# Kernel optimization log

Measured on AMD Instinct MI355X. Metric: run time of the kernel, lower is better.

## Reference

```python
import jax, jax.numpy as jnp
import numpy as np
import math

DIM = 1024
NUM_HEADS = 16
HEAD_DIM = DIM // NUM_HEADS  # 64
LAYER_IDX = 12
LAMBDA_INIT = 0.8 - 0.6 * math.exp(-0.3 * (LAYER_IDX - 1))
LN_EPS = 1e-5


def setup_inputs() -> dict:
    key = jax.random.key(0)
    ks = jax.random.split(key, 11)
    B, S = 2, 2048
    x = jax.random.normal(ks[0], (B, S, DIM), dtype=jnp.float32)
    s = 1.0 / math.sqrt(DIM)
    Wq = jax.random.normal(ks[1], (DIM, 2 * DIM), dtype=jnp.float32) * s
    Wk = jax.random.normal(ks[2], (DIM, 2 * DIM), dtype=jnp.float32) * s
    Wv = jax.random.normal(ks[3], (DIM, DIM), dtype=jnp.float32) * s
    Wo = jax.random.normal(ks[4], (DIM, DIM), dtype=jnp.float32) * s
    lambda_q1 = jax.random.normal(ks[5], (HEAD_DIM,), dtype=jnp.float32) * 0.1
    lambda_k1 = jax.random.normal(ks[6], (HEAD_DIM,), dtype=jnp.float32) * 0.1
    lambda_q2 = jax.random.normal(ks[7], (HEAD_DIM,), dtype=jnp.float32) * 0.1
    lambda_k2 = jax.random.normal(ks[8], (HEAD_DIM,), dtype=jnp.float32) * 0.1
    gamma = jnp.ones((DIM,), dtype=jnp.float32)
    beta = jnp.zeros((DIM,), dtype=jnp.float32)
    return {"x": x, "Wq": Wq, "Wk": Wk, "Wv": Wv, "Wo": Wo,
            "lambda_q1": lambda_q1, "lambda_k1": lambda_k1,
            "lambda_q2": lambda_q2, "lambda_k2": lambda_k2,
            "gamma": gamma, "beta": beta}


def reference(x, Wq, Wk, Wv, Wo, lambda_q1, lambda_k1, lambda_q2, lambda_k2, gamma, beta):
    B, S, _ = x.shape
    scaling = HEAD_DIM ** (-0.5)
    # projections: [B,S,H,2d] / [B,S,H,d] -> [B,H,S,*]
    Q = (x @ Wq).reshape(B, S, NUM_HEADS, 2 * HEAD_DIM).transpose(0, 2, 1, 3)
    K = (x @ Wk).reshape(B, S, NUM_HEADS, 2 * HEAD_DIM).transpose(0, 2, 1, 3)
    V = (x @ Wv).reshape(B, S, NUM_HEADS, HEAD_DIM).transpose(0, 2, 1, 3)
    # lambda scalar
    lamb = (jnp.exp(jnp.sum(lambda_q1 * lambda_k1))
            - jnp.exp(jnp.sum(lambda_q2 * lambda_k2)) + LAMBDA_INIT)
    Q1, Q2 = jnp.split(Q, 2, axis=-1)
    K1, K2 = jnp.split(K, 2, axis=-1)
    A1 = jnp.einsum('bhqd,bhkd->bhqk', Q1, K1) * scaling
    A2 = jnp.einsum('bhqd,bhkd->bhqk', Q2, K2) * scaling
    attn = jax.nn.softmax(A1, axis=-1) - lamb * jax.nn.softmax(A2, axis=-1)
    out = jnp.einsum('bhqk,bhkd->bhqd', attn, V)  # [B,H,S,d]
    out = out.transpose(0, 2, 1, 3).reshape(B, S, DIM)
    out = out @ Wo
    # LayerNorm
    mu = jnp.mean(out, axis=-1, keepdims=True)
    var = jnp.var(out, axis=-1, keepdims=True)
    out = (out - mu) * jax.lax.rsqrt(var + LN_EPS) * gamma + beta
    return out
```

## Files before the change

### kernel.cpp

```cpp
#include <hip/hip_runtime.h>
#include <hip/hip_bf16.h>

typedef short bf16x8 __attribute__((ext_vector_type(8)));
typedef float f32x4 __attribute__((ext_vector_type(4)));
typedef unsigned short us4v __attribute__((ext_vector_type(4)));
typedef unsigned int uint2v __attribute__((ext_vector_type(2)));

#define DEV static __device__ __forceinline__

DEV float bf2f(unsigned short u){ unsigned int x = ((unsigned int)u)<<16; float f; __builtin_memcpy(&f,&x,4); return f; }
DEV unsigned short f2bf(float f){ unsigned int x; __builtin_memcpy(&x,&f,4); x = (x + 0x7fffu + ((x>>16)&1u)) >> 16; return (unsigned short)x; }

DEV unsigned int pack_trunc(float lo, float hi){
  unsigned int a, b;
  __builtin_memcpy(&a, &lo, 4);
  __builtin_memcpy(&b, &hi, 4);
  return (b & 0xffff0000u) | (a >> 16);
}

DEV void stor(unsigned short* p, float v){ *p = f2bf(v); }
DEV void stor(float* p, float v){ *p = v; }

#if __has_builtin(__builtin_amdgcn_permlane32_swap)
DEV uint2v pl32(unsigned int a, unsigned int b){ return __builtin_amdgcn_permlane32_swap(a, b, false, false); }
#else
DEV uint2v pl32(unsigned int a, unsigned int b){
  unsigned int sa = (unsigned int)__shfl_xor((int)a, 32);
  unsigned int sb = (unsigned int)__shfl_xor((int)b, 32);
  bool hi = (threadIdx.x & 32) != 0;
  uint2v r; r[0] = hi ? sb : a; r[1] = hi ? b : sa; return r;
}
#endif
#if __has_builtin(__builtin_amdgcn_permlane16_swap)
DEV uint2v pl16(unsigned int a, unsigned int b){ return __builtin_amdgcn_permlane16_swap(a, b, false, false); }
#else
DEV uint2v pl16(unsigned int a, unsigned int b){
  unsigned int sa = (unsigned int)__shfl_xor((int)a, 16);
  unsigned int sb = (unsigned int)__shfl_xor((int)b, 16);
  bool hi = (threadIdx.x & 16) != 0;
  uint2v r; r[0] = hi ? sb : a; r[1] = hi ? b : sa; return r;
}
#endif

#define GLOAD_LDS16(gptr, lptr) \
  __builtin_amdgcn_global_load_lds((__attribute__((address_space(1))) void*)(gptr), \
      (__attribute__((address_space(3))) void*)(lptr), 16, 0, 0)

template<typename OutT>
__global__ __launch_bounds__(256) void gemm_bt(
    const unsigned short* __restrict__ A,
    const unsigned short* __restrict__ Bt,
    OutT* __restrict__ C, int M, int N, int K)
{
  __shared__ unsigned short As[128*32];
  __shared__ unsigned short Bs[128*32];
  const int tid = threadIdx.x;
  const int w = tid>>6, l = tid&63, g = l>>4, q = l&15;
  const int m0 = blockIdx.x*128, n0 = blockIdx.y*128;
  f32x4 acc[4][4];
  const f32x4 fz = {0.f,0.f,0.f,0.f};
  for (int i=0;i<4;i++) for(int j=0;j<4;j++) acc[i][j] = fz;
  for (int k0 = 0; k0 < K; k0 += 32) {
    __syncthreads();
    #pragma unroll
    for (int r = 0; r < 2; ++r) {
      int p = r*4096 + tid*16;
      int row = p>>6, colb = p&63;
      const char* ga = (const char*)(A  + (size_t)(m0+row)*K + k0) + colb;
      const char* gb = (const char*)(Bt + (size_t)(n0+row)*K + k0) + colb;
      GLOAD_LDS16(ga, (char*)As + r*4096 + w*1024);
      GLOAD_LDS16(gb, (char*)Bs + r*4096 + w*1024);
    }
    __syncthreads();
    bf16x8 af[4], bfr[4];
    #pragma unroll
    for (int i=0;i<4;i++){
      af[i]  = *(const bf16x8*)&As[((w>>1)*64 + i*16 + q)*32 + g*8];
      bfr[i] = *(const bf16x8*)&Bs[((w&1)*64 + i*16 + q)*32 + g*8];
    }
    #pragma unroll
    for (int i=0;i<4;i++)
      #pragma unroll
      for (int j=0;j<4;j++)
        acc[i][j] = __builtin_amdgcn_mfma_f32_16x16x32_bf16(af[i], bfr[j], acc[i][j], 0,0,0);
  }
  #pragma unroll
  for (int i=0;i<4;i++)
    #pragma unroll
    for (int j=0;j<4;j++)
      #pragma unroll
      for (int v=0;v<4;v++){
        int row = m0 + (w>>1)*64 + i*16 + g*4 + v;
        int col = n0 + (w&1)*64 + j*16 + q;
        stor(&C[(size_t)row*N + col], acc[i][j][v]);
      }
}

__global__ __launch_bounds__(256,2) void diff_attn(
    const unsigned short* __restrict__ Qp,
    const unsigned short* __restrict__ Kp,
    const unsigned short* __restrict__ Vt,
    const float* __restrict__ lambp,
    unsigned short* __restrict__ aout)
{
  const int LDQ = 5120;
  __shared__ unsigned short Ks[2][64*128];
  __shared__ unsigned short Vs[2][64*64];
  const int tid = threadIdx.x, w = tid>>6, l = tid&63, g = l>>4, q = l&15;
  const int qb = blockIdx.x, h = blockIdx.y, b = blockIdx.z;
  const int qrow0 = b*2048 + qb*128 + w*32;
  const f32x4 fz = {0.f,0.f,0.f,0.f};
  const short one_bf = (short)0x3f80;
  const bf16x8 ones = {one_bf,one_bf,one_bf,one_bf,one_bf,one_bf,one_bf,one_bf};

  const float QSCALE = 0.125f * 1.4426950408889634f;
  bf16x8 q1f[2][2], q2f[2][2];
  #pragma unroll
  for (int qh=0; qh<2; ++qh){
    const unsigned short* qp = Qp + (size_t)(qrow0 + qh*16 + q)*LDQ + h*128;
    #pragma unroll
    for (int kf=0;kf<2;kf++){
      bf16x8 t1 = *(const bf16x8*)(qp + kf*32 + g*8);
      bf16x8 t2 = *(const bf16x8*)(qp + 64 + kf*32 + g*8);
      #pragma unroll
      for (int e=0;e<8;e++){
        t1[e] = (short)f2bf(bf2f((unsigned short)t1[e]) * QSCALE);
        t2[e] = (short)f2bf(bf2f((unsigned short)t2[e]) * QSCALE);
      }
      q1f[qh][kf]=t1; q2f[qh][kf]=t2;
    }
  }
  f32x4 acc1[2][4], acc2[2][4];
  f32x4 acc_s1[2], acc_s2[2];
  #pragma unroll
  for (int qh=0;qh<2;qh++){
    acc_s1[qh]=fz; acc_s2[qh]=fz;
    #pragma unroll
    for (int i=0;i<4;i++){ acc1[qh][i]=fz; acc2[qh][i]=fz; }
  }

  const int rowl = l;
  const int swl = rowl & 7;
  const unsigned short* pK = Kp + (size_t)(b*2048 + rowl)*LDQ + h*128;
  const unsigned short* pV = Vt + (size_t)(h*64 + rowl)*4096 + b*2048;

  bf16x8 kreg[4], vreg[2];
  auto LOADT = [&](){
    #pragma unroll
    for (int c=0;c<4;c++) kreg[c] = *(const bf16x8*)(pK + (w + c*4)*8);
    #pragma unroll
    for (int c=0;c<2;c++) vreg[c] = *(const bf16x8*)(pV + (w + c*4)*8);
    pK += (size_t)64*LDQ;
    pV += 64;
  };
  auto WRITET = [&](int bb){
    #pragma unroll
    for (int c=0;c<4;c++){
      int ch = w + c*4;
      *(bf16x8*)&Ks[bb][rowl*128 + (ch^swl)*8] = kreg[c];
    }
    #pragma unroll
    for (int c=0;c<2;c++){
      int ch = w + c*4;
      *(bf16x8*)&Vs[bb][rowl*64 + (ch^swl)*8] = vreg[c];
    }
  };

  LOADT();
  WRITET(0);
  __syncthreads();

  for (int t=0; t<32; ++t) {
    const int bb = t & 1;
    if (t < 31) LOADT();
    const int sw = q & 7;

    unsigned int c1[2][4][2], c2[2][4][2];
    #pragma unroll
    for (int fn=0; fn<4; ++fn) {
      const unsigned short* kr = &Ks[bb][(fn*16 + q)*128];
      bf16x8 kb0 = *(const bf16x8*)&kr[((0+g)^sw)*8];
      bf16x8 kb1 = *(const bf16x8*)&kr[((4+g)^sw)*8];
      bf16x8 kc0 = *(const bf16x8*)&kr[((8+g)^sw)*8];
      bf16x8 kc1 = *(const bf16x8*)&kr[((12+g)^sw)*8];
      f32x4 za[2], zc[2];
      __builtin_amdgcn_s_setprio(1);
      #pragma unroll
      for (int qh=0; qh<2; ++qh){
        f32x4 a = fz, c = fz;
        a = __builtin_amdgcn_mfma_f32_16x16x32_bf16(kb0, q1f[qh][0], a, 0,0,0);
        a = __builtin_amdgcn_mfma_f32_16x16x32_bf16(kb1, q1f[qh][1], a, 0,0,0);
        c = __builtin_amdgcn_mfma_f32_16x16x32_bf16(kc0, q2f[qh][0], c, 0,0,0);
        c = __builtin_amdgcn_mfma_f32_16x16x32_bf16(kc1, q2f[qh][1], c, 0,0,0);
        za[qh]=a; zc[qh]=c;
      }
      __builtin_amdgcn_s_setprio(0);
      #pragma unroll
      for (int qh=0; qh<2; ++qh){
        float e0 = exp2f(za[qh][0]), e1 = exp2f(za[qh][1]);
        float e2 = exp2f(za[qh][2]), e3 = exp2f(za[qh][3]);
        c1[qh][fn][0] = pack_trunc(e0,e1); c1[qh][fn][1] = pack_trunc(e2,e3);
        float f0 = exp2f(zc[qh][0]), f1 = exp2f(zc[qh][1]);
        float f2 = exp2f(zc[qh][2]), f3 = exp2f(zc[qh][3]);
        c2[qh][fn][0] = pack_trunc(f0,f1); c2[qh][fn][1] = pack_trunc(f2,f3);
      }
    }

    bf16x8 pa1[2][2], pa2[2][2];
    #pragma unroll
    for (int qh=0; qh<2; ++qh)
      #pragma unroll
      for (int kh=0; kh<2; ++kh){
        unsigned int* u1 = (unsigned int*)&pa1[qh][kh];
        unsigned int* u2 = (unsigned int*)&pa2[qh][kh];
        #pragma unroll
        for (int j=0;j<2;j++){
          uint2v d = pl32(c1[qh][2*kh][j], c1[qh][2*kh+1][j]);
          uint2v e = pl16(d[0], d[1]);
          u1[j] = e[0]; u1[2+j] = e[1];
          uint2v d2 = pl32(c2[qh][2*kh][j], c2[qh][2*kh+1][j]);
          uint2v e2 = pl16(d2[0], d2[1]);
          u2[j] = e2[0]; u2[2+j] = e2[1];
        }
      }

    __builtin_amdgcn_s_setprio(1);
    #pragma unroll
    for (int kh=0; kh<2; ++kh){
      #pragma unroll
      for (int qh=0; qh<2; ++qh){
        acc_s1[qh] = __builtin_amdgcn_mfma_f32_16x16x32_bf16(pa1[qh][kh], ones, acc_s1[qh], 0,0,0);
        acc_s2[qh] = __builtin_amdgcn_mfma_f32_16x16x32_bf16(pa2[qh][kh], ones, acc_s2[qh], 0,0,0);
      }
      #pragma unroll
      for (int fd=0; fd<4; ++fd){
        bf16x8 vb = *(const bf16x8*)&Vs[bb][(fd*16+q)*64 + ((kh*4+g)^sw)*8];
        #pragma unroll
        for (int qh=0; qh<2; ++qh){
          acc1[qh][fd] = __builtin_amdgcn_mfma_f32_16x16x32_bf16(pa1[qh][kh], vb, acc1[qh][fd], 0,0,0);
          acc2[qh][fd] = __builtin_amdgcn_mfma_f32_16x16x32_bf16(pa2[qh][kh], vb, acc2[qh][fd], 0,0,0);
        }
      }
    }
    __builtin_amdgcn_s_setprio(0);

    if (t < 31){
      WRITET((t+1)&1);
      __syncthreads();
    }
  }

  float lamb = lambp[0];
  #pragma unroll
  for (int qh=0; qh<2; ++qh){
    float inv1[4], inv2[4];
    #pragma unroll
    for (int i=0;i<4;i++){
      inv1[i] = 1.0f/acc_s1[qh][i];
      inv2[i] = lamb/acc_s2[qh][i];
    }
    #pragma unroll
    for (int fd=0; fd<4; ++fd)
      #pragma unroll
      for (int i=0;i<4;i++){
        float val = acc1[qh][fd][i]*inv1[i] - acc2[qh][fd][i]*inv2[i];
        int row = qrow0 + qh*16 + g*4 + i;
        int col = h*64 + fd*16 + q;
        aout[(size_t)row*1024 + col] = f2bf(val);
      }
  }
}

__global__ __launch_bounds__(256) void f32_to_bf16_k(const float* __restrict__ in, unsigned short* __restrict__ out, int n){
  int i = (blockIdx.x*256 + threadIdx.x)*4;
  if (i >= n) return;
  float4 vv = *(const float4*)(in + i);
  us4v o; o[0]=f2bf(vv.x); o[1]=f2bf(vv.y); o[2]=f2bf(vv.z); o[3]=f2bf(vv.w);
  *(us4v*)(out + i) = o;
}

__global__ void transpose_f32_bf16(const float* __restrict__ in, unsigned short* __restrict__ out, int R, int C){
  __shared__ unsigned short t[32][33];
  int c0 = blockIdx.x*32, r0 = blockIdx.y*32;
  int x = threadIdx.x, y = threadIdx.y;
  #pragma unroll
  for (int d=0; d<32; d+=8) t[y+d][x] = f2bf(in[(size_t)(r0+y+d)*C + c0 + x]);
  __syncthreads();
  #pragma unroll
  for (int d=0; d<32; d+=8) out[(size_t)(c0+y+d)*R + r0 + x] = t[x][y+d];
}

__global__ void transpose_bf16_ld(const unsigned short* __restrict__ in, unsigned short* __restrict__ out, int R, int C, int ldin){
  __shared__ unsigned short t[32][33];
  int c0 = blockIdx.x*32, r0 = blockIdx.y*32;
  int x = threadIdx.x, y = threadIdx.y;
  #pragma unroll
  for (int d=0; d<32; d+=8) t[y+d][x] = in[(size_t)(r0+y+d)*ldin + c0 + x];
  __syncthreads();
  #pragma unroll
  for (int d=0; d<32; d+=8) out[(size_t)(c0+y+d)*R + r0 + x] = t[x][y+d];
}

__global__ void lamb_k(const float* lq1, const float* lk1, const float* lq2, const float* lk2, float* out){
  int i = threadIdx.x;
  float a = lq1[i]*lk1[i], c = lq2[i]*lk2[i];
  #pragma unroll
  for (int o=32;o>0;o>>=1){ a += __shfl_down(a,o); c += __shfl_down(c,o); }
  if (i==0) out[0] = expf(a) - expf(c) + 0.7778700995592560f;
}

__global__ __launch_bounds__(256) void ln_k(const float* __restrict__ in, const float* __restrict__ gam,
                                            const float* __restrict__ bet, float* __restrict__ out){
  int row = blockIdx.x, t = threadIdx.x;
  const float4* rp = (const float4*)(in + (size_t)row*1024);
  float4 v4 = rp[t];
  float s = v4.x+v4.y+v4.z+v4.w;
  float ss = v4.x*v4.x+v4.y*v4.y+v4.z*v4.z+v4.w*v4.w;
  #pragma unroll
  for (int o=1;o<64;o<<=1){ s += __shfl_xor(s,o); ss += __shfl_xor(ss,o); }
  __shared__ float red[8];
  int w = t>>6, l = t&63;
  if (l==0){ red[w]=s; red[4+w]=ss; }
  __syncthreads();
  s = red[0]+red[1]+red[2]+red[3];
  ss = red[4]+red[5]+red[6]+red[7];
  float mean = s*(1.0f/1024.0f);
  float var = ss*(1.0f/1024.0f) - mean*mean;
  float rstd = rsqrtf(var + 1e-5f);
  float4 gv = ((const float4*)gam)[t], bv = ((const float4*)bet)[t];
  float4 o;
  o.x = (v4.x-mean)*rstd*gv.x + bv.x;
  o.y = (v4.y-mean)*rstd*gv.y + bv.y;
  o.z = (v4.z-mean)*rstd*gv.z + bv.z;
  o.w = (v4.w-mean)*rstd*gv.w + bv.w;
  ((float4*)(out + (size_t)row*1024))[t] = o;
}

extern "C" void kernel_launch(void* const* d_in, const int* in_sizes, int n_in,
                              void* d_out, int out_size, void* d_ws, size_t ws_size,
                              hipStream_t stream) {
  const float* x     = (const float*)d_in[0];
  const float* Wq    = (const float*)d_in[1];
  const float* Wk    = (const float*)d_in[2];
  const float* Wv    = (const float*)d_in[3];
  const float* Wo    = (const float*)d_in[4];
  const float* lq1   = (const float*)d_in[5];
  const float* lk1   = (const float*)d_in[6];
  const float* lq2   = (const float*)d_in[7];
  const float* lk2   = (const float*)d_in[8];
  const float* gamma = (const float*)d_in[9];
  const float* beta  = (const float*)d_in[10];
  float* out = (float*)d_out;

  char* ws = (char*)d_ws;
  unsigned short* xb    = (unsigned short*)(ws);
  unsigned short* WcatT = (unsigned short*)(ws + 8388608);
  unsigned short* WoT   = (unsigned short*)(ws + 18874368);
  unsigned short* QKV   = (unsigned short*)(ws + 20971520);
  unsigned short* Vtb   = (unsigned short*)(ws + 62914560);
  unsigned short* AOb   = (unsigned short*)(ws + 71303168);
  float*          proj  = (float*)(ws + 79691776);
  float*          lambp = (float*)(ws + 96468992);

  dim3 tb(32,8);
  f32_to_bf16_k<<<4096, 256, 0, stream>>>(x, xb, 4194304);
  transpose_f32_bf16<<<dim3(64,32), tb, 0, stream>>>(Wq, WcatT,             1024, 2048);
  transpose_f32_bf16<<<dim3(64,32), tb, 0, stream>>>(Wk, WcatT + 2048*1024, 1024, 2048);
  transpose_f32_bf16<<<dim3(32,32), tb, 0, stream>>>(Wv, WcatT + 4096*1024, 1024, 1024);
  transpose_f32_bf16<<<dim3(32,32), tb, 0, stream>>>(Wo, WoT, 1024, 1024);
  lamb_k<<<1, 64, 0, stream>>>(lq1, lk1, lq2, lk2, lambp);

  gemm_bt<unsigned short><<<dim3(32,40), 256, 0, stream>>>(xb, WcatT, QKV, 4096, 5120, 1024);
  transpose_bf16_ld<<<dim3(32,128), tb, 0, stream>>>(QKV + 4096, Vtb, 4096, 1024, 5120);

  diff_attn<<<dim3(16,16,2), 256, 0, stream>>>(QKV, QKV + 2048, Vtb, lambp, AOb);

  gemm_bt<float><<<dim3(32,8), 256, 0, stream>>>(AOb, WoT, proj, 4096, 1024, 1024);
  ln_k<<<4096, 256, 0, stream>>>(proj, gamma, beta, out);
}
```

Measured before the change: 231.1 us.

## Stage K/V tiles via direct global-to-LDS loads and fold Q scale into Wq

Replaces register-staged K/V tile loads and explicit LDS writes in the attention kernel with direct global-to-LDS loads using swizzled source addresses, removing the staging registers and the separate write pass. The softmax scale is folded into the Wq conversion, so the attention kernel no longer rescales Q. The exp2 calls switch to the hardware builtin. This risks slightly different rounding and depends on the swizzle mapping of the direct loads matching the readers.

```diff
diff --git a/kernel.cpp b/kernel.cpp
--- a/kernel.cpp
+++ b/kernel.cpp
@@ -20,6 +20,12 @@
 
 DEV void stor(unsigned short* p, float v){ *p = f2bf(v); }
 DEV void stor(float* p, float v){ *p = v; }
+
+#if __has_builtin(__builtin_amdgcn_exp2f)
+DEV float fexp2(float x){ return __builtin_amdgcn_exp2f(x); }
+#else
+DEV float fexp2(float x){ return exp2f(x); }
+#endif
 
 #if __has_builtin(__builtin_amdgcn_permlane32_swap)
 DEV uint2v pl32(unsigned int a, unsigned int b){ return __builtin_amdgcn_permlane32_swap(a, b, false, false); }
@@ -108,26 +114,20 @@
   __shared__ unsigned short Vs[2][64*64];
   const int tid = threadIdx.x, w = tid>>6, l = tid&63, g = l>>4, q = l&15;
   const int qb = blockIdx.x, h = blockIdx.y, b = blockIdx.z;
-  const int qrow0 = b*2048 + qb*128 + w*32;
+  const int b2048 = b*2048;
+  const int qrow0 = b2048 + qb*128 + w*32;
   const f32x4 fz = {0.f,0.f,0.f,0.f};
   const short one_bf = (short)0x3f80;
   const bf16x8 ones = {one_bf,one_bf,one_bf,one_bf,one_bf,one_bf,one_bf,one_bf};
 
-  const float QSCALE = 0.125f * 1.4426950408889634f;
   bf16x8 q1f[2][2], q2f[2][2];
   #pragma unroll
   for (int qh=0; qh<2; ++qh){
     const unsigned short* qp = Qp + (size_t)(qrow0 + qh*16 + q)*LDQ + h*128;
     #pragma unroll
     for (int kf=0;kf<2;kf++){
-      bf16x8 t1 = *(const bf16x8*)(qp + kf*32 + g*8);
-      bf16x8 t2 = *(const bf16x8*)(qp + 64 + kf*32 + g*8);
-      #pragma unroll
-      for (int e=0;e<8;e++){
-        t1[e] = (short)f2bf(bf2f((unsigned short)t1[e]) * QSCALE);
-        t2[e] = (short)f2bf(bf2f((unsigned short)t2[e]) * QSCALE);
-      }
-      q1f[qh][kf]=t1; q2f[qh][kf]=t2;
+      q1f[qh][kf] = *(const bf16x8*)(qp + kf*32 + g*8);
+      q2f[qh][kf] = *(const bf16x8*)(qp + 64 + kf*32 + g*8);
     }
   }
   f32x4 acc1[2][4], acc2[2][4];
@@ -139,40 +139,29 @@
     for (int i=0;i<4;i++){ acc1[qh][i]=fz; acc2[qh][i]=fz; }
   }
 
-  const int rowl = l;
-  const int swl = rowl & 7;
-  const unsigned short* pK = Kp + (size_t)(b*2048 + rowl)*LDQ + h*128;
-  const unsigned short* pV = Vt + (size_t)(h*64 + rowl)*4096 + b*2048;
-
-  bf16x8 kreg[4], vreg[2];
-  auto LOADT = [&](){
-    #pragma unroll
-    for (int c=0;c<4;c++) kreg[c] = *(const bf16x8*)(pK + (w + c*4)*8);
-    #pragma unroll
-    for (int c=0;c<2;c++) vreg[c] = *(const bf16x8*)(pV + (w + c*4)*8);
-    pK += (size_t)64*LDQ;
-    pV += 64;
+  auto STAGE = [&](int bb, int kt){
+    #pragma unroll
+    for (int ii=0; ii<4; ++ii){
+      int krow = w*16 + ii*4 + (l>>4);
+      int gr = (l&15) ^ (krow&7);
+      const unsigned short* src = Kp + (size_t)(b2048 + kt + krow)*LDQ + h*128 + gr*8;
+      GLOAD_LDS16(src, (char*)&Ks[bb][0] + (w*16 + ii*4)*256);
+    }
+    #pragma unroll
+    for (int jj=0; jj<2; ++jj){
+      int vrow = w*16 + jj*8 + (l>>3);
+      int gr = (l&7) ^ (vrow&7);
+      const unsigned short* src = Vt + (size_t)(h*64 + vrow)*4096 + b2048 + kt + gr*8;
+      GLOAD_LDS16(src, (char*)&Vs[bb][0] + (w*16 + jj*8)*128);
+    }
   };
-  auto WRITET = [&](int bb){
-    #pragma unroll
-    for (int c=0;c<4;c++){
-      int ch = w + c*4;
-      *(bf16x8*)&Ks[bb][rowl*128 + (ch^swl)*8] = kreg[c];
-    }
-    #pragma unroll
-    for (int c=0;c<2;c++){
-      int ch = w + c*4;
-      *(bf16x8*)&Vs[bb][rowl*64 + (ch^swl)*8] = vreg[c];
-    }
-  };
-
-  LOADT();
-  WRITET(0);
+
+  STAGE(0, 0);
   __syncthreads();
 
   for (int t=0; t<32; ++t) {
     const int bb = t & 1;
-    if (t < 31) LOADT();
+    if (t < 31) STAGE(bb^1, (t+1)*64);
     const int sw = q & 7;
 
     unsigned int c1[2][4][2], c2[2][4][2];
@@ -197,11 +186,11 @@
       __builtin_amdgcn_s_setprio(0);
       #pragma unroll
       for (int qh=0; qh<2; ++qh){
-        float e0 = exp2f(za[qh][0]), e1 = exp2f(za[qh][1]);
-        float e2 = exp2f(za[qh][2]), e3 = exp2f(za[qh][3]);
+        float e0 = fexp2(za[qh][0]), e1 = fexp2(za[qh][1]);
+        float e2 = fexp2(za[qh][2]), e3 = fexp2(za[qh][3]);
         c1[qh][fn][0] = pack_trunc(e0,e1); c1[qh][fn][1] = pack_trunc(e2,e3);
-        float f0 = exp2f(zc[qh][0]), f1 = exp2f(zc[qh][1]);
-        float f2 = exp2f(zc[qh][2]), f3 = exp2f(zc[qh][3]);
+        float f0 = fexp2(zc[qh][0]), f1 = fexp2(zc[qh][1]);
+        float f2 = fexp2(zc[qh][2]), f3 = fexp2(zc[qh][3]);
         c2[qh][fn][0] = pack_trunc(f0,f1); c2[qh][fn][1] = pack_trunc(f2,f3);
       }
     }
@@ -244,10 +233,7 @@
     }
     __builtin_amdgcn_s_setprio(0);
 
-    if (t < 31){
-      WRITET((t+1)&1);
-      __syncthreads();
-    }
+    if (t < 31) __syncthreads();
   }
 
   float lamb = lambp[0];
@@ -279,12 +265,12 @@
   *(us4v*)(out + i) = o;
 }
 
-__global__ void transpose_f32_bf16(const float* __restrict__ in, unsigned short* __restrict__ out, int R, int C){
+__global__ void transpose_f32_bf16(const float* __restrict__ in, unsigned short* __restrict__ out, int R, int C, float scale){
   __shared__ unsigned short t[32][33];
   int c0 = blockIdx.x*32, r0 = blockIdx.y*32;
   int x = threadIdx.x, y = threadIdx.y;
   #pragma unroll
-  for (int d=0; d<32; d+=8) t[y+d][x] = f2bf(in[(size_t)(r0+y+d)*C + c0 + x]);
+  for (int d=0; d<32; d+=8) t[y+d][x] = f2bf(in[(size_t)(r0+y+d)*C + c0 + x] * scale);
   __syncthreads();
   #pragma unroll
   for (int d=0; d<32; d+=8) out[(size_t)(c0+y+d)*R + r0 + x] = t[x][y+d];
@@ -362,12 +348,13 @@
   float*          proj  = (float*)(ws + 79691776);
   float*          lambp = (float*)(ws + 96468992);
 
+  const float QSCALE = 0.125f * 1.4426950408889634f;
   dim3 tb(32,8);
   f32_to_bf16_k<<<4096, 256, 0, stream>>>(x, xb, 4194304);
-  transpose_f32_bf16<<<dim3(64,32), tb, 0, stream>>>(Wq, WcatT,             1024, 2048);
-  transpose_f32_bf16<<<dim3(64,32), tb, 0, stream>>>(Wk, WcatT + 2048*1024, 1024, 2048);
-  transpose_f32_bf16<<<dim3(32,32), tb, 0, stream>>>(Wv, WcatT + 4096*1024, 1024, 1024);
-  transpose_f32_bf16<<<dim3(32,32), tb, 0, stream>>>(Wo, WoT, 1024, 1024);
+  transpose_f32_bf16<<<dim3(64,32), tb, 0, stream>>>(Wq, WcatT,             1024, 2048, QSCALE);
+  transpose_f32_bf16<<<dim3(64,32), tb, 0, stream>>>(Wk, WcatT + 2048*1024, 1024, 2048, 1.0f);
+  transpose_f32_bf16<<<dim3(32,32), tb, 0, stream>>>(Wv, WcatT + 4096*1024, 1024, 1024, 1.0f);
+  transpose_f32_bf16<<<dim3(32,32), tb, 0, stream>>>(Wo, WoT, 1024, 1024, 1.0f);
   lamb_k<<<1, 64, 0, stream>>>(lq1, lk1, lq2, lk2, lambp);
 
   gemm_bt<unsigned short><<<dim3(32,40), 256, 0, stream>>>(xb, WcatT, QKV, 4096, 5120, 1024);
```

Measured after the change: 201.7 us. 12.7% less time.
